# Optimization experiments

Measured on AMD Instinct MI355X. Metric: run time of the kernel, lower is better.

## Reference

```python
import jax, jax.numpy as jnp
import numpy as np
import math

B, N, D, H_HEADS, DFF = 4, 1024, 512, 16, 2048
DH = D // H_HEADS  # 32
FACTOR = 0.5 / math.sqrt(DH)
EPS = 1e-5

def layer_norm(x, g, b):
    m = jnp.mean(x, axis=-1, keepdims=True)
    v = jnp.var(x, axis=-1, keepdims=True)
    return (x - m) * jax.lax.rsqrt(v + EPS) * g + b

def setup_inputs() -> dict:
    key = jax.random.key(0)
    ks = jax.random.split(key, 24)
    s = 0.02
    inp = {
        'H': jax.random.normal(ks[0], (B, N, D), jnp.float32),
        'V': jax.random.normal(ks[1], (B, N, 3, D), jnp.float32),
        'mask': jnp.ones((B, N), dtype=bool),
        'rbf_bias': jax.random.normal(ks[2], (B, 1, N, N), jnp.float32),
        'attn_bias_param': jnp.zeros((1, H_HEADS, 1, 1), jnp.float32),
        'Wq': jax.random.normal(ks[3], (4 * D, D), jnp.float32) * s,
        'bq': jnp.zeros((4 * D,), jnp.float32),
        'Wk': jax.random.normal(ks[4], (4 * D, D), jnp.float32) * s,
        'bk': jnp.zeros((4 * D,), jnp.float32),
        'Wv': jax.random.normal(ks[5], (D, D), jnp.float32) * s,
        'bv': jnp.zeros((D,), jnp.float32),
        'Wvv': jax.random.normal(ks[6], (D, D), jnp.float32) * s,
        'Wo': jax.random.normal(ks[7], (D, D), jnp.float32) * s,
        'bo': jnp.zeros((D,), jnp.float32),
        'Wvo': jax.random.normal(ks[8], (D, D), jnp.float32) * s,
        'ln1_g': jnp.ones((D,), jnp.float32), 'ln1_b': jnp.zeros((D,), jnp.float32),
        'ln2_g': jnp.ones((D,), jnp.float32), 'ln2_b': jnp.zeros((D,), jnp.float32),
        'Wlv': jax.random.normal(ks[9], (2 * D, D), jnp.float32) * s,
        'W1': jax.random.normal(ks[10], (DFF, 2 * D), jnp.float32) * s,
        'b1': jnp.zeros((DFF,), jnp.float32),
        'W2': jax.random.normal(ks[11], (2 * D, DFF), jnp.float32) * s,
        'b2': jnp.zeros((2 * D,), jnp.float32),
    }
    return inp

def _forward(H, V, mask, rbf_bias, attn_bias_param, Wq, bq, Wk, bk, Wv, bv, Wvv,
             Wo, bo, Wvo, ln1_g, ln1_b, ln2_g, ln2_b, Wlv, W1, b1, W2, b2):
    H_res, V_res = H, V
    # pre-LN for attention
    H_norm = layer_norm(H, ln1_g, ln1_b)
    # q/k: (B,N,h,4*dh); scalar v: (B,N,h,dh)
    Hq = (H_norm @ Wq.T + bq).reshape(B, N, H_HEADS, 4 * DH)
    Hk = (H_norm @ Wk.T + bk).reshape(B, N, H_HEADS, 4 * DH)
    Hv = (H_norm @ Wv.T + bv).reshape(B, N, H_HEADS, DH)
    # vector value: (B,N,3,D) -> (B,N,3,h,dh) -> (B,N,h,3,dh) -> (B,N,h,3*dh)
    Vv = (V @ Wvv.T).reshape(B, N, 3, H_HEADS, DH)
    Vv = jnp.swapaxes(Vv, -2, -3).reshape(B, N, H_HEADS, 3 * DH)
    V_attn = jnp.concatenate([Hv, Vv], axis=-1)  # (B,N,h,4*dh)
    # bias + mask: bias (B,h,N,N) via broadcast; mask over keys
    bias = rbf_bias + attn_bias_param
    neg_inf = jnp.array(-jnp.inf, bias.dtype)
    bias = jnp.where(mask[:, None, None, :], bias, neg_inf)
    logits = jnp.einsum('bnhd,bmhd->bhnm', Hq, Hk) * FACTOR + bias
    attn = jax.nn.softmax(logits, axis=-1)
    res = jnp.einsum('bhnm,bmhd->bnhd', attn, V_attn)  # (B,N,h,4*dh)
    H_r = res[..., :DH].reshape(B, N, D)
    V_r = res[..., DH:].reshape(B, N, H_HEADS, 3, DH)
    V_r = jnp.swapaxes(V_r, -2, -3).reshape(B, N, 3, D)
    H_o = H_r @ Wo.T + bo
    V_o = V_r @ Wvo.T
    H = H_res + H_o
    V = V_res + V_o
    # GVP FFN (pre-LN, vector_act='none')
    H_ffn_res, V_ffn_res = H, V
    H_in = layer_norm(H, ln2_g, ln2_b)
    V_proj = V @ Wlv.T  # (B,N,3,2D)
    V1, V2 = V_proj[..., :D], V_proj[..., D:]
    v1_norm = jnp.linalg.norm(V1, axis=-2)  # (B,N,D)
    scaler = jnp.concatenate([H_in, v1_norm], axis=-1)  # (B,N,2D)
    h1 = jax.nn.silu(scaler @ W1.T + b1)
    scaler_out = h1 @ W2.T + b2  # (B,N,2D)
    H_out, V_update = scaler_out[..., :D], scaler_out[..., D:]
    V_out = V_update[..., None, :] * V2  # (B,N,3,D)
    H = H_ffn_res + H_out
    V = V_ffn_res + V_out
    return H, V

def reference(H, V, mask, rbf_bias, attn_bias_param, Wq, bq, Wk, bk, Wv, bv, Wvv,
              Wo, bo, Wvo, ln1_g, ln1_b, ln2_g, ln2_b, Wlv, W1, b1, W2, b2):
    return _forward(H, V, mask, rbf_bias, attn_bias_param, Wq, bq, Wk, bk, Wv, bv,
                    Wvv, Wo, bo, Wvo, ln1_g, ln1_b, ln2_g, ln2_b, Wlv, W1, b1, W2, b2)
```

## Files before the change

kernel.cpp:

```cpp
#include <hip/hip_runtime.h>
#include <hip/hip_bf16.h>

#define B_   4
#define N_   1024
#define D_   512
#define HH   16
#define DFF_ 2048

typedef __bf16 bf16;
typedef __bf16 bf16x8 __attribute__((ext_vector_type(8)));
typedef __bf16 bf16x4 __attribute__((ext_vector_type(4)));
typedef float  f32x4  __attribute__((ext_vector_type(4)));
typedef _Float16 f16x8 __attribute__((ext_vector_type(8)));
typedef unsigned short ushort8 __attribute__((ext_vector_type(8)));

#define MFMA16(a,b,c) __builtin_amdgcn_mfma_f32_16x16x32_bf16((a),(b),(c),0,0,0)

#define GLOAD16(gp, lp) __builtin_amdgcn_global_load_lds( \
    (const __attribute__((address_space(1))) void*)(gp),  \
    (__attribute__((address_space(3))) void*)(lp), 16, 0, 0)

#define LOG2E 1.44269504088896f

static __device__ __forceinline__ float bf2f(bf16 x){ return (float)x; }
static __device__ __forceinline__ bf16  f2bf(float x){ return (bf16)x; }
static __device__ __forceinline__ bf16x4 pack4(f32x4 v){
  bf16x4 o = { f2bf(v[0]), f2bf(v[1]), f2bf(v[2]), f2bf(v[3]) };
  return o;
}

struct ConvTab {
  const float* src[10];
  bf16*        dst[10];
  int          n8[10];
};

__global__ __launch_bounds__(256) void k_convert(ConvTab t)
{
  int gid = blockIdx.x * 256 + threadIdx.x;
  int gsz = gridDim.x * 256;
  for (int s = 0; s < 10; ++s) {
    const float4* src = (const float4*)t.src[s];
    bf16x8* dst = (bf16x8*)t.dst[s];
    int n8 = t.n8[s];
    for (int i = gid; i < n8; i += gsz) {
      float4 a = src[i * 2], b = src[i * 2 + 1];
      bf16x8 o = { f2bf(a.x), f2bf(a.y), f2bf(a.z), f2bf(a.w),
                   f2bf(b.x), f2bf(b.y), f2bf(b.z), f2bf(b.w) };
      dst[i] = o;
    }
  }
}

__global__ __launch_bounds__(256)
void k_rbffrag(const float* __restrict__ rbf, _Float16* __restrict__ out,
               const float* __restrict__ bq, const float* __restrict__ bk,
               const float* __restrict__ bv, float* __restrict__ bqkv)
{
  const int blk = blockIdx.x;
  const int gi = blk * 256 + threadIdx.x;
  if (gi < 4608)
    bqkv[gi] = (gi < 2048) ? bq[gi] : ((gi < 4096) ? bk[gi - 2048] : bv[gi - 4096]);
  const int kt = blk & 31;
  const int qt = (blk >> 5) & 15;
  const int b  = blk >> 9;
  const int tid = threadIdx.x;
  const int lane = tid & 63, w = tid >> 6;
  const int l15 = lane & 15, l4 = lane >> 4;
  const float* src = rbf + ((size_t)b << 20)
                   + (size_t)(qt * 64 + w * 16 + l4 * 4) * 1024 + kt * 32 + l15;
  f16x8 v;
  #pragma unroll
  for (int nf = 0; nf < 2; ++nf)
    #pragma unroll
    for (int r = 0; r < 4; ++r)
      v[nf * 4 + r] = (_Float16)(src[(size_t)r * 1024 + nf * 16] * LOG2E);
  *(f16x8*)(out + ((size_t)blk * 256 + tid) * 8) = v;
}

static __device__ __forceinline__
void ln_body(const float* __restrict__ x, const float* __restrict__ g,
             const float* __restrict__ b, bf16* __restrict__ out, int ldo, int bid)
{
  int w = threadIdx.x >> 6, lane = threadIdx.x & 63;
  int row = bid * 4 + w;
  const float* xr = x + (size_t)row * D_;
  float4 v0 = *(const float4*)(xr + lane * 8);
  float4 v1 = *(const float4*)(xr + lane * 8 + 4);
  float s  = v0.x + v0.y + v0.z + v0.w + v1.x + v1.y + v1.z + v1.w;
  float sq = v0.x*v0.x + v0.y*v0.y + v0.z*v0.z + v0.w*v0.w
           + v1.x*v1.x + v1.y*v1.y + v1.z*v1.z + v1.w*v1.w;
  #pragma unroll
  for (int d = 1; d < 64; d <<= 1) { s += __shfl_xor(s, d); sq += __shfl_xor(sq, d); }
  float mean = s * (1.f / D_);
  float var  = sq * (1.f / D_) - mean * mean;
  float rs = rsqrtf(var + 1e-5f);
  float4 g0 = *(const float4*)(g + lane*8), g1 = *(const float4*)(g + lane*8 + 4);
  float4 b0 = *(const float4*)(b + lane*8), b1 = *(const float4*)(b + lane*8 + 4);
  bf16x4 o0 = { f2bf((v0.x-mean)*rs*g0.x + b0.x), f2bf((v0.y-mean)*rs*g0.y + b0.y),
                f2bf((v0.z-mean)*rs*g0.z + b0.z), f2bf((v0.w-mean)*rs*g0.w + b0.w) };
  bf16x4 o1 = { f2bf((v1.x-mean)*rs*g1.x + b1.x), f2bf((v1.y-mean)*rs*g1.y + b1.y),
                f2bf((v1.z-mean)*rs*g1.z + b1.z), f2bf((v1.w-mean)*rs*g1.w + b1.w) };
  *(bf16x4*)(out + (size_t)row * ldo + lane * 8)     = o0;
  *(bf16x4*)(out + (size_t)row * ldo + lane * 8 + 4) = o1;
}

__global__ __launch_bounds__(256)
void k_ln(const float* __restrict__ x, const float* __restrict__ g,
          const float* __restrict__ b, bf16* __restrict__ out, int ldo)
{
  ln_body(x, g, b, out, ldo, blockIdx.x);
}

static __device__ __forceinline__
void vnorm_body(const bf16* __restrict__ vproj, bf16* __restrict__ scaler, int bid)
{
  const int idx = bid * 256 + threadIdx.x;
  const int m = idx >> 7, d4 = (idx & 127) * 4;
  float a0 = 0, a1 = 0, a2 = 0, a3 = 0;
  #pragma unroll
  for (int t = 0; t < 3; ++t) {
    ushort4 u = *(const ushort4*)((const unsigned short*)vproj + ((size_t)(m * 3 + t)) * 1024 + d4);
    float x0 = bf2f(__builtin_bit_cast(bf16, u.x));
    float x1 = bf2f(__builtin_bit_cast(bf16, u.y));
    float x2 = bf2f(__builtin_bit_cast(bf16, u.z));
    float x3 = bf2f(__builtin_bit_cast(bf16, u.w));
    a0 += x0 * x0; a1 += x1 * x1; a2 += x2 * x2; a3 += x3 * x3;
  }
  bf16x4 ov = { f2bf(sqrtf(a0)), f2bf(sqrtf(a1)), f2bf(sqrtf(a2)), f2bf(sqrtf(a3)) };
  *(bf16x4*)(scaler + (size_t)m * 1024 + 512 + d4) = ov;
}

__global__ __launch_bounds__(256)
void k_ln2vnorm(const float* __restrict__ x, const float* __restrict__ g,
                const float* __restrict__ b, bf16* __restrict__ scaler,
                const bf16* __restrict__ vproj)
{
  int bid = blockIdx.x;
  if (bid < 1024) ln_body(x, g, b, scaler, 1024, bid);
  else            vnorm_body(vproj, scaler, bid - 1024);
}

struct EpiArgs {
  const float* bias;
  const float* res;
  const float* res2;
  float*       outf;
  bf16*        outb;
  bf16*        outb2;
  bf16*        outb3;
  const float* hnew;
  const bf16*  vnewb;
  const bf16*  vproj;
  float*       outH;
  float*       outV;
  const bf16*  Bw2;
};

template<int EPI, int ALOAD>
__device__ __forceinline__
void gemm_body(const bf16* __restrict__ A, const bf16* __restrict__ Bw,
               int N, int K, const EpiArgs& ea, int by, int bx, char* sm)
{
  const int tid  = threadIdx.x;
  const int lane = tid & 63;
  const int w    = tid >> 6;
  const int l15 = lane & 15, l4 = lane >> 4;
  const int wr = w >> 1, wc = w & 1;
  const size_t row0 = (size_t)by * 128;
  const int    col0 = bx * 128;

  const int g  = (lane & 3) ^ ((lane >> 4) & 3);
  const int rl = (lane >> 2);

  const char* Ab8 = (const char*)A;
  const char* Bb8 = (const char*)Bw;
  if constexpr (ALOAD == 3) { if (row0 >= 4096) Bb8 = (const char*)ea.Bw2; }

  auto gaddrA = [&](int r, int kt) -> const char* {
    if constexpr (ALOAD == 0) {
      return Ab8 + (((row0 + r) * (size_t)K) + (size_t)kt * 32 + g * 8) * 2;
    } else {
      int m = (int)row0 + r;
      if (row0 < 4096) {
        int b = m >> 10, q = m & 1023;
        return Ab8 + ((((size_t)(b * 16 + kt)) * 1024 + q) * 128 + g * 8) * 2;
      } else {
        int m2 = m - 4096;
        int b = m2 / 3072; int rem = m2 - b * 3072;
        int q = rem / 3; int t = rem - q * 3;
        return Ab8 + ((((size_t)(b * 16 + kt)) * 1024 + q) * 128 + 32 + t * 32 + g * 8) * 2;
      }
    }
  };
  auto gaddrB = [&](int r, int kt) -> const char* {
    return Bb8 + (((size_t)(col0 + r) * K) + (size_t)kt * 32 + g * 8) * 2;
  };

  auto stage = [&](int bufc, int kt) {
    #pragma unroll
    for (int j = 0; j < 2; ++j) {
      const int r = (w + 4 * j) * 16 + rl;
      char* lb = sm + bufc * 16384 + (w + 4 * j) * 1024;
      GLOAD16(gaddrA(r, kt), lb);
      GLOAD16(gaddrB(r, kt), lb + 8192);
    }
  };

  f32x4 acc[4][4] = {};
  const int nk = K >> 5;
  const int sw = (l15 >> 2) & 3;
  const int cofs = (l4 ^ sw) * 16;

  auto compute = [&](int bufc) {
    const char* Abase = sm + bufc * 16384;
    const char* Bbase = Abase + 8192;
    bf16x8 af[4], bfr[4];
    #pragma unroll
    for (int i = 0; i < 4; ++i) {
      af[i]  = *(const bf16x8*)(Abase + (wr * 64 + i * 16 + l15) * 64 + cofs);
      bfr[i] = *(const bf16x8*)(Bbase + (wc * 64 + i * 16 + l15) * 64 + cofs);
    }
    #pragma unroll
    for (int i = 0; i < 4; ++i)
      #pragma unroll
      for (int j = 0; j < 4; ++j)
        acc[i][j] = MFMA16(bfr[j], af[i], acc[i][j]);
  };

  stage(0, 0);
  stage(1, 1);
  int b0 = 0, b1 = 1, b2 = 2;
  for (int kt = 0; kt < nk; ++kt) {
    if (kt + 1 < nk) { asm volatile("s_waitcnt vmcnt(4)" ::: "memory"); }
    else             { asm volatile("s_waitcnt vmcnt(0)" ::: "memory"); }
    __builtin_amdgcn_sched_barrier(0);
    __builtin_amdgcn_s_barrier();
    __builtin_amdgcn_sched_barrier(0);
    compute(b0);
    if (kt + 2 < nk) stage(b2, kt + 2);
    int t = b0; b0 = b1; b1 = b2; b2 = t;
  }

  const int mb0 = (int)row0 + wr * 64 + l15;
  const int nb0 = col0 + wc * 64 + l4 * 4;

  const float* biasp = ea.bias;
  if constexpr (EPI == 8) { if (row0 >= 4096) biasp = nullptr; }
  float4 bias4[4];
  #pragma unroll
  for (int j = 0; j < 4; ++j)
    bias4[j] = biasp ? *(const float4*)(biasp + nb0 + j * 16) : make_float4(0, 0, 0, 0);

  #pragma unroll
  for (int i = 0; i < 4; ++i) {
    const int row = mb0 + i * 16;
    #pragma unroll
    for (int j = 0; j < 4; ++j) {
      const int nb = nb0 + j * 16;
      f32x4 v = acc[i][j];
      v[0] += bias4[j].x; v[1] += bias4[j].y; v[2] += bias4[j].z; v[3] += bias4[j].w;
      if constexpr (EPI == 0) {
        *(bf16x4*)(ea.outb + (size_t)row * N + nb) = pack4(v);
      } else if constexpr (EPI == 2) {
        int q = row / 3, t = row - q * 3;
        int colp = ((nb >> 5) << 7) + 32 + t * 32 + (nb & 31);
        *(bf16x4*)(ea.outb + (size_t)q * 2048 + colp) = pack4(v);
      } else if constexpr (EPI == 5) {
        #pragma unroll
        for (int r = 0; r < 4; ++r) v[r] = v[r] / (1.f + __expf(-v[r]));
        *(bf16x4*)(ea.outb + (size_t)row * N + nb) = pack4(v);
      } else if constexpr (EPI == 7) {
        if (col0 < 2048) {
          *(bf16x4*)(ea.outb + (size_t)row * 2048 + nb) = pack4(v);
        } else if (col0 < 4096) {
          *(bf16x4*)(ea.outb2 + (size_t)row * 2048 + nb - 2048) = pack4(v);
        } else {
          int colv = nb - 4096;
          int colp = ((colv >> 5) << 7) | (colv & 31);
          *(bf16x4*)(ea.outb3 + (size_t)row * 2048 + colp) = pack4(v);
        }
      } else if constexpr (EPI == 8) {
        if (row0 < 4096) {
          size_t idx = (size_t)row * 512 + nb;
          float4 r4 = *(const float4*)(ea.res + idx);
          float4 o4 = make_float4(r4.x + v[0], r4.y + v[1], r4.z + v[2], r4.w + v[3]);
          *(float4*)(ea.outf + idx) = o4;
        } else {
          size_t idx = (size_t)(row - 4096) * 512 + nb;
          float4 r4 = *(const float4*)(ea.res2 + idx);
          f32x4 o; o[0] = r4.x + v[0]; o[1] = r4.y + v[1]; o[2] = r4.z + v[2]; o[3] = r4.w + v[3];
          *(bf16x4*)(ea.outb + idx) = pack4(o);
        }
      } else {
        if (col0 < 512) {
          size_t idx = (size_t)row * 512 + nb;
          float4 h4 = *(const float4*)(ea.hnew + idx);
          float4 o4 = make_float4(h4.x + v[0], h4.y + v[1], h4.z + v[2], h4.w + v[3]);
          *(float4*)(ea.outH + idx) = o4;
        } else {
          int colv = nb - 512;
          #pragma unroll
          for (int t = 0; t < 3; ++t) {
            size_t vi = ((size_t)row * 3 + t) * 512 + colv;
            bf16x4 vn = *(const bf16x4*)(ea.vnewb + vi);
            bf16x4 vp = *(const bf16x4*)(ea.vproj + ((size_t)row * 3 + t) * 1024 + nb);
            float4 o4 = make_float4(bf2f(vn[0]) + v[0] * bf2f(vp[0]),
                                    bf2f(vn[1]) + v[1] * bf2f(vp[1]),
                                    bf2f(vn[2]) + v[2] * bf2f(vp[2]),
                                    bf2f(vn[3]) + v[3] * bf2f(vp[3]));
            *(float4*)(ea.outV + vi) = o4;
          }
        }
      }
    }
  }
}

template<int EPI, int ALOAD>
__global__ __launch_bounds__(256)
void k_gemm(const bf16* __restrict__ A, const bf16* __restrict__ Bw,
            int N, int K, EpiArgs ea)
{
  __shared__ char sm[3][16384];
  gemm_body<EPI, ALOAD>(A, Bw, N, K, ea, blockIdx.y, blockIdx.x, &sm[0][0]);
}

__global__ __launch_bounds__(256)
void k_gemm_qkvv(const bf16* __restrict__ Aq, const bf16* __restrict__ Bq,
                 const bf16* __restrict__ Av, const bf16* __restrict__ Bv,
                 EpiArgs e7, EpiArgs e2)
{
  __shared__ char sm[3][16384];
  int bid = blockIdx.x;
  if (bid < 1152) {
    gemm_body<7, 0>(Aq, Bq, 4608, 512, e7, bid / 36, bid % 36, &sm[0][0]);
  } else {
    int i = bid - 1152;
    gemm_body<2, 0>(Av, Bv, 512, 512, e2, i >> 2, i & 3, &sm[0][0]);
  }
}

__global__ __launch_bounds__(256)
void k_transpose(const bf16* __restrict__ in, bf16* __restrict__ out)
{
  __shared__ unsigned short t[64][65];
  const int blk = blockIdx.x;
  const int bh = blk >> 5;
  const int dt = (blk >> 4) & 1;
  const int nt = blk & 15;
  const int b = bh >> 4, h = bh & 15;
  const int n0 = nt * 64, d0 = dt * 64;
  const unsigned short* ip = (const unsigned short*)in;
  unsigned short* op = (unsigned short*)out;

  const int nr = threadIdx.x >> 2;
  const int c0 = (threadIdx.x & 3) * 16;
  const unsigned short* src = ip + ((size_t)(b * N_ + n0 + nr)) * 2048 + h * 128 + d0 + c0;
  ushort8 va = *(const ushort8*)(src);
  ushort8 vb = *(const ushort8*)(src + 8);
  #pragma unroll
  for (int j = 0; j < 8; ++j) { t[nr][c0 + j] = va[j]; t[nr][c0 + 8 + j] = vb[j]; }
  __syncthreads();
  const int dr = threadIdx.x >> 2;
  const int nb = (threadIdx.x & 3) * 16;
  ushort8 oa, ob;
  #pragma unroll
  for (int j = 0; j < 8; ++j) { oa[j] = t[nb + j][dr]; ob[j] = t[nb + 8 + j][dr]; }
  unsigned short* dst = op + ((size_t)(bh * 128 + d0 + dr)) * N_ + n0 + nb;
  *(ushort8*)(dst) = oa;
  *(ushort8*)(dst + 8) = ob;
}

__global__ __launch_bounds__(256, 2)
void k_attn(const bf16* __restrict__ Hq, const bf16* __restrict__ Hk,
            const bf16* __restrict__ VT, const _Float16* __restrict__ rbfF,
            const float* __restrict__ abp, bf16* __restrict__ O)
{
  __shared__ bf16 Kl[2][32 * 128];
  __shared__ bf16 Vl[2][128 * 32];
  __shared__ bf16 Pl[4][32 * 38];

  const int blk = blockIdx.x;
  const int inner = blk & 7;
  const int outer = blk >> 3;
  const int b    = inner >> 1;
  const int h    = (inner & 1) * 8 + (outer >> 3);
  const int qt   = outer & 7;
  const int q0   = qt * 128;
  const int tid = threadIdx.x;
  const int lane = tid & 63;
  const int w = tid >> 6;
  const int l15 = lane & 15, l4 = lane >> 4;

  bf16x8 qf[2][4];
  #pragma unroll
  for (int qa = 0; qa < 2; ++qa) {
    const bf16* qptr = Hq + ((size_t)(b * N_ + q0 + w * 32 + qa * 16 + l15)) * 2048 + h * 128;
    #pragma unroll
    for (int kk = 0; kk < 4; ++kk) qf[qa][kk] = *(const bf16x8*)(qptr + kk * 32 + l4 * 8);
  }

  const float ab8 = (abp[h] - 8.f) * LOG2E;
  const float c1  = 0.08838834764831845f * LOG2E;
  f32x4 o[2][8] = {};
  float lr[2][4] = {};

  const bf16* kbase = Hk + ((size_t)b * N_) * 2048 + h * 128;
  const bf16* vbase = VT + ((size_t)((b * HH + h) * 128)) * N_;
  const _Float16* rbase[2];
  #pragma unroll
  for (int qa = 0; qa < 2; ++qa) {
    const int fb = 2 * w + qa;
    const int qt64 = qt * 2 + (fb >> 2);
    const int tidf = (fb & 3) * 64 + lane;
    rbase[qa] = rbfF + ((size_t)(b * 16 + qt64) * 32) * 2048 + (size_t)tidf * 8;
  }

  const int kr_l = lane >> 4;
  const int vr_l = lane >> 2;

  auto stage = [&](int bi, int kt) {
    const int k0 = kt * 32;
    #pragma unroll
    for (int i = 0; i < 2; ++i) {
      const int kr = (i * 4 + w) * 4 + kr_l;
      const int ks = (lane & 15) ^ (kr & 7);
      GLOAD16(kbase + (size_t)(k0 + kr) * 2048 + ks * 8, &Kl[bi][(i * 4 + w) * 512]);
      const int vr = (i * 4 + w) * 16 + vr_l;
      const int vs = (lane & 3) ^ ((vr >> 1) & 3);
      GLOAD16(vbase + (size_t)vr * N_ + k0 + vs * 8, &Vl[bi][(i * 4 + w) * 512]);
    }
  };

  stage(0, 0);
  f16x8 rf_n[2] = { *(const f16x8*)rbase[0], *(const f16x8*)rbase[1] };
  __syncthreads();

  const int vslot = (l4 ^ ((l15 >> 1) & 3)) * 8;

  auto tile = [&](int bufc, int kt) {
    f16x8 rf[2] = { rf_n[0], rf_n[1] };
    if (kt + 1 < 32) {
      stage(bufc ^ 1, kt + 1);
      rf_n[0] = *(const f16x8*)(rbase[0] + (size_t)(kt + 1) * 2048);
      rf_n[1] = *(const f16x8*)(rbase[1] + (size_t)(kt + 1) * 2048);
    }
    f32x4 s[2][2];
    __builtin_amdgcn_s_setprio(1);
    #pragma unroll
    for (int nf = 0; nf < 2; ++nf) {
      f32x4 a0 = {}, a1 = {};
      #pragma unroll
      for (int kk = 0; kk < 4; ++kk) {
        bf16x8 kf = *(const bf16x8*)(&Kl[bufc][(nf * 16 + l15) * 128 +
                                               (((kk * 4 + l4) ^ (l15 & 7)) * 8)]);
        a0 = MFMA16(qf[0][kk], kf, a0);
        a1 = MFMA16(qf[1][kk], kf, a1);
      }
      s[0][nf] = a0; s[1][nf] = a1;
    }
    __builtin_amdgcn_s_setprio(0);
    #pragma unroll
    for (int qa = 0; qa < 2; ++qa)
      #pragma unroll
      for (int nf = 0; nf < 2; ++nf)
        #pragma unroll
        for (int r = 0; r < 4; ++r) {
          float p = __builtin_amdgcn_exp2f(s[qa][nf][r] * c1 +
                                           ((float)rf[qa][nf * 4 + r] + ab8));
          lr[qa][r] += p;
          Pl[w][(qa * 16 + l4 * 4 + r) * 38 + nf * 16 + l15] = f2bf(p);
        }
    bf16x8 pf[2];
    #pragma unroll
    for (int qa = 0; qa < 2; ++qa)
      pf[qa] = *(const bf16x8*)(&Pl[w][(qa * 16 + l15) * 38 + l4 * 8]);
    __builtin_amdgcn_s_setprio(1);
    #pragma unroll
    for (int of = 0; of < 8; ++of) {
      bf16x8 vf = *(const bf16x8*)(&Vl[bufc][(of * 16 + l15) * 32 + vslot]);
      o[0][of] = MFMA16(pf[0], vf, o[0][of]);
      o[1][of] = MFMA16(pf[1], vf, o[1][of]);
    }
    __builtin_amdgcn_s_setprio(0);
    __syncthreads();
  };

  for (int kt = 0; kt < 32; kt += 2) {
    tile(0, kt);
    tile(1, kt + 1);
  }

  #pragma unroll
  for (int qa = 0; qa < 2; ++qa) {
    #pragma unroll
    for (int d = 1; d < 16; d <<= 1)
      #pragma unroll
      for (int r = 0; r < 4; ++r) lr[qa][r] += __shfl_xor(lr[qa][r], d);
  }

  #pragma unroll
  for (int qa = 0; qa < 2; ++qa) {
    float inv[4];
    #pragma unroll
    for (int r = 0; r < 4; ++r) inv[r] = 1.f / lr[qa][r];
    bf16* obase = O + (((size_t)(b * HH + h) * 1024) + q0 + w * 32 + qa * 16 + l4 * 4) * 128;
    #pragma unroll
    for (int of = 0; of < 8; ++of) {
      #pragma unroll
      for (int r = 0; r < 4; ++r)
        obase[(size_t)r * 128 + of * 16 + l15] = f2bf(o[qa][of][r] * inv[r]);
    }
  }
}

extern "C" void kernel_launch(void* const* d_in, const int* in_sizes, int n_in,
                              void* d_out, int out_size, void* d_ws, size_t ws_size,
                              hipStream_t stream)
{
  (void)in_sizes; (void)n_in; (void)out_size; (void)ws_size;
  const float* H   = (const float*)d_in[0];
  const float* V   = (const float*)d_in[1];
  const float* rbf = (const float*)d_in[3];
  const float* abp = (const float*)d_in[4];
  const float* Wq  = (const float*)d_in[5];
  const float* bq  = (const float*)d_in[6];
  const float* Wk  = (const float*)d_in[7];
  const float* bk  = (const float*)d_in[8];
  const float* Wv  = (const float*)d_in[9];
  const float* bv  = (const float*)d_in[10];
  const float* Wvv = (const float*)d_in[11];
  const float* Wo  = (const float*)d_in[12];
  const float* bo  = (const float*)d_in[13];
  const float* Wvo = (const float*)d_in[14];
  const float* g1  = (const float*)d_in[15];
  const float* be1 = (const float*)d_in[16];
  const float* g2  = (const float*)d_in[17];
  const float* be2 = (const float*)d_in[18];
  const float* Wlv = (const float*)d_in[19];
  const float* W1  = (const float*)d_in[20];
  const float* b1  = (const float*)d_in[21];
  const float* W2  = (const float*)d_in[22];
  const float* b2  = (const float*)d_in[23];

  char* ws = (char*)d_ws;
  size_t off = 0;
  auto alloc = [&](size_t bytes) -> char* {
    char* p = ws + off;
    off += (bytes + 255) & ~(size_t)255;
    return p;
  };
  bf16* wWq   = (bf16*)alloc((size_t)2048 * 512 * 2);
  bf16* wWk   = (bf16*)alloc((size_t)2048 * 512 * 2);
  bf16* wWv   = (bf16*)alloc((size_t)512 * 512 * 2);
  bf16* wWvv  = (bf16*)alloc((size_t)512 * 512 * 2);
  bf16* wWo   = (bf16*)alloc((size_t)512 * 512 * 2);
  bf16* wWvo  = (bf16*)alloc((size_t)512 * 512 * 2);
  bf16* wWlv  = (bf16*)alloc((size_t)1024 * 512 * 2);
  bf16* wW1   = (bf16*)alloc((size_t)2048 * 1024 * 2);
  bf16* wW2   = (bf16*)alloc((size_t)1024 * 2048 * 2);
  bf16* wV    = (bf16*)alloc((size_t)12288 * 512 * 2);
  bf16* wHn   = (bf16*)alloc((size_t)4096 * 512 * 2);
  bf16* wHq   = (bf16*)alloc((size_t)4096 * 2048 * 2);
  bf16* wHk   = (bf16*)alloc((size_t)4096 * 2048 * 2);
  bf16* wVat  = (bf16*)alloc((size_t)4096 * 2048 * 2);
  bf16* wVT   = (bf16*)alloc((size_t)4096 * 2048 * 2);
  bf16* wO    = (bf16*)alloc((size_t)4096 * 2048 * 2);
  float* wHnew = (float*)alloc((size_t)4096 * 512 * 4);
  float* bqkv  = (float*)alloc((size_t)4608 * 4);
  bf16* wVproj  = wHq;
  bf16* wScaler = wVat;
  bf16* wH1     = wVT;
  _Float16* rbfF = (_Float16*)wHnew;
  float* outH = (float*)d_out;
  float* outV = outH + (size_t)4096 * 512;

  ConvTab ct;
  const float* csrc[10] = {Wq, Wk, Wv, Wvv, Wo, Wvo, Wlv, W1, W2, V};
  bf16* cdst[10] = {wWq, wWk, wWv, wWvv, wWo, wWvo, wWlv, wW1, wW2, wV};
  const int cn[10] = {2048*512, 2048*512, 512*512, 512*512, 512*512, 512*512,
                      1024*512, 2048*1024, 1024*2048, 12288*512};
  for (int i = 0; i < 10; ++i) { ct.src[i] = csrc[i]; ct.dst[i] = cdst[i]; ct.n8[i] = cn[i] / 8; }
  k_convert<<<2048, 256, 0, stream>>>(ct);
  k_rbffrag<<<2048, 256, 0, stream>>>(rbf, rbfF, bq, bk, bv, bqkv);

  k_ln<<<1024, 256, 0, stream>>>(H, g1, be1, wHn, 512);

  EpiArgs e7{}, e2{}, ea{};
  e7.bias = bqkv; e7.outb = wHq; e7.outb2 = wHk; e7.outb3 = wVat;
  e2.outb = wVat;
  k_gemm_qkvv<<<1536, 256, 0, stream>>>(wHn, wWq, wV, wWvv, e7, e2);

  k_transpose<<<2048, 256, 0, stream>>>(wVat, wVT);

  k_attn<<<512, 256, 0, stream>>>(wHq, wHk, wVT, rbfF, abp, wO);

  ea = {}; ea.bias = bo; ea.res = H; ea.res2 = V; ea.outf = wHnew; ea.outb = wV; ea.Bw2 = wWvo;
  k_gemm<8,3><<<dim3(4, 128), 256, 0, stream>>>(wO, wWo, 512, 512, ea);

  ea = {}; ea.outb = wVproj;
  k_gemm<0,0><<<dim3(8, 96), 256, 0, stream>>>(wV, wWlv, 1024, 512, ea);

  k_ln2vnorm<<<3072, 256, 0, stream>>>(wHnew, g2, be2, wScaler, wVproj);

  ea = {}; ea.bias = b1; ea.outb = wH1;
  k_gemm<5,0><<<dim3(16, 32), 256, 0, stream>>>(wScaler, wW1, 2048, 1024, ea);

  ea = {}; ea.bias = b2; ea.hnew = wHnew; ea.vnewb = wV; ea.vproj = wVproj;
  ea.outH = outH; ea.outV = outV;
  k_gemm<6,0><<<dim3(8, 32), 256, 0, stream>>>(wH1, wW2, 1024, 2048, ea);
}
```

Before: 248.8 us.

## Merge front-end prep kernels and reorder GEMM block traversal

Folds the weight conversion, rbf fragment packing, and first layer norm into one launch, which removes two kernel launches and the idle gaps between them. Every GEMM grid is now linearised with the row-tile index varying fastest, so consecutive blocks share the same weight column tile. The goal is better L2 reuse of the weights, at the risk of poorer reuse of the activation tiles.

```diff
diff --git a/kernel.cpp b/kernel.cpp
--- a/kernel.cpp
+++ b/kernel.cpp
@@ -35,10 +35,11 @@
   int          n8[10];
 };
 
-__global__ __launch_bounds__(256) void k_convert(ConvTab t)
-{
-  int gid = blockIdx.x * 256 + threadIdx.x;
-  int gsz = gridDim.x * 256;
+static __device__ __forceinline__
+void conv_body(const ConvTab& t, int bid)
+{
+  int gid = bid * 256 + threadIdx.x;
+  const int gsz = 2048 * 256;
   for (int s = 0; s < 10; ++s) {
     const float4* src = (const float4*)t.src[s];
     bf16x8* dst = (bf16x8*)t.dst[s];
@@ -52,12 +53,11 @@
   }
 }
 
-__global__ __launch_bounds__(256)
-void k_rbffrag(const float* __restrict__ rbf, _Float16* __restrict__ out,
-               const float* __restrict__ bq, const float* __restrict__ bk,
-               const float* __restrict__ bv, float* __restrict__ bqkv)
-{
-  const int blk = blockIdx.x;
+static __device__ __forceinline__
+void rbffrag_body(const float* __restrict__ rbf, _Float16* __restrict__ out,
+                  const float* __restrict__ bq, const float* __restrict__ bk,
+                  const float* __restrict__ bv, float* __restrict__ bqkv, int blk)
+{
   const int gi = blk * 256 + threadIdx.x;
   if (gi < 4608)
     bqkv[gi] = (gi < 2048) ? bq[gi] : ((gi < 4096) ? bk[gi - 2048] : bv[gi - 4096]);
@@ -106,10 +106,16 @@
 }
 
 __global__ __launch_bounds__(256)
-void k_ln(const float* __restrict__ x, const float* __restrict__ g,
-          const float* __restrict__ b, bf16* __restrict__ out, int ldo)
-{
-  ln_body(x, g, b, out, ldo, blockIdx.x);
+void k_front(ConvTab t, const float* __restrict__ rbf, _Float16* __restrict__ rbfF,
+             const float* __restrict__ bq, const float* __restrict__ bk,
+             const float* __restrict__ bv, float* __restrict__ bqkv,
+             const float* __restrict__ H, const float* __restrict__ g1,
+             const float* __restrict__ be1, bf16* __restrict__ hn)
+{
+  int bid = blockIdx.x;
+  if (bid < 2048)      conv_body(t, bid);
+  else if (bid < 4096) rbffrag_body(rbf, rbfF, bq, bk, bv, bqkv, bid - 2048);
+  else                 ln_body(H, g1, be1, hn, 512, bid - 4096);
 }
 
 static __device__ __forceinline__
@@ -320,10 +326,12 @@
 template<int EPI, int ALOAD>
 __global__ __launch_bounds__(256)
 void k_gemm(const bf16* __restrict__ A, const bf16* __restrict__ Bw,
-            int N, int K, EpiArgs ea)
+            int N, int K, int ny, EpiArgs ea)
 {
   __shared__ char sm[3][16384];
-  gemm_body<EPI, ALOAD>(A, Bw, N, K, ea, blockIdx.y, blockIdx.x, &sm[0][0]);
+  int bid = blockIdx.x;
+  int by = bid % ny, bx = bid / ny;
+  gemm_body<EPI, ALOAD>(A, Bw, N, K, ea, by, bx, &sm[0][0]);
 }
 
 __global__ __launch_bounds__(256)
@@ -334,10 +342,10 @@
   __shared__ char sm[3][16384];
   int bid = blockIdx.x;
   if (bid < 1152) {
-    gemm_body<7, 0>(Aq, Bq, 4608, 512, e7, bid / 36, bid % 36, &sm[0][0]);
+    gemm_body<7, 0>(Aq, Bq, 4608, 512, e7, bid & 31, bid >> 5, &sm[0][0]);
   } else {
     int i = bid - 1152;
-    gemm_body<2, 0>(Av, Bv, 512, 512, e2, i >> 2, i & 3, &sm[0][0]);
+    gemm_body<2, 0>(Av, Bv, 512, 512, e2, i % 96, i / 96, &sm[0][0]);
   }
 }
 
@@ -582,10 +590,7 @@
   const int cn[10] = {2048*512, 2048*512, 512*512, 512*512, 512*512, 512*512,
                       1024*512, 2048*1024, 1024*2048, 12288*512};
   for (int i = 0; i < 10; ++i) { ct.src[i] = csrc[i]; ct.dst[i] = cdst[i]; ct.n8[i] = cn[i] / 8; }
-  k_convert<<<2048, 256, 0, stream>>>(ct);
-  k_rbffrag<<<2048, 256, 0, stream>>>(rbf, rbfF, bq, bk, bv, bqkv);
-
-  k_ln<<<1024, 256, 0, stream>>>(H, g1, be1, wHn, 512);
+  k_front<<<5120, 256, 0, stream>>>(ct, rbf, rbfF, bq, bk, bv, bqkv, H, g1, be1, wHn);
 
   EpiArgs e7{}, e2{}, ea{};
   e7.bias = bqkv; e7.outb = wHq; e7.outb2 = wHk; e7.outb3 = wVat;
@@ -597,17 +602,17 @@
   k_attn<<<512, 256, 0, stream>>>(wHq, wHk, wVT, rbfF, abp, wO);
 
   ea = {}; ea.bias = bo; ea.res = H; ea.res2 = V; ea.outf = wHnew; ea.outb = wV; ea.Bw2 = wWvo;
-  k_gemm<8,3><<<dim3(4, 128), 256, 0, stream>>>(wO, wWo, 512, 512, ea);
+  k_gemm<8,3><<<512, 256, 0, stream>>>(wO, wWo, 512, 512, 128, ea);
 
   ea = {}; ea.outb = wVproj;
-  k_gemm<0,0><<<dim3(8, 96), 256, 0, stream>>>(wV, wWlv, 1024, 512, ea);
+  k_gemm<0,0><<<768, 256, 0, stream>>>(wV, wWlv, 1024, 512, 96, ea);
 
   k_ln2vnorm<<<3072, 256, 0, stream>>>(wHnew, g2, be2, wScaler, wVproj);
 
   ea = {}; ea.bias = b1; ea.outb = wH1;
-  k_gemm<5,0><<<dim3(16, 32), 256, 0, stream>>>(wScaler, wW1, 2048, 1024, ea);
+  k_gemm<5,0><<<512, 256, 0, stream>>>(wScaler, wW1, 2048, 1024, 32, ea);
 
   ea = {}; ea.bias = b2; ea.hnew = wHnew; ea.vnewb = wV; ea.vproj = wVproj;
   ea.outH = outH; ea.outV = outV;
-  k_gemm<6,0><<<dim3(8, 32), 256, 0, stream>>>(wH1, wW2, 1024, 2048, ea);
-}
+  k_gemm<6,0><<<256, 256, 0, stream>>>(wH1, wW2, 1024, 2048, 32, ea);
+}
```

New measurement: 236.9 us, median of 2. 4.8% less time.
